# Kernel optimization log

Measured on AMD Instinct MI355X. Metric: run time of the kernel, lower is better.

The kernel has to match this reference:

```python
import jax, jax.numpy as jnp
import numpy as np
import math

B, T, C = 2, 2048, 2048
NH, L = 16, 128  # n_head, LCompression


def setup_inputs() -> dict:
    key = jax.random.key(0)
    ks = jax.random.split(key, 7)
    s = 0.02
    return {
        "x": jax.random.normal(ks[0], (B, T, C), dtype=jnp.float32),
        # latent: Linear(n_embd -> LComp), stored as [in, out]
        "W_lat": jax.random.normal(ks[1], (C, L), dtype=jnp.float32) * s,
        "b_lat": jnp.zeros((L,), dtype=jnp.float32),
        # Wd: Linear(n_embd -> n_head*LComp)
        "W_d": jax.random.normal(ks[2], (C, NH * L), dtype=jnp.float32) * s,
        "b_d": jnp.zeros((NH * L,), dtype=jnp.float32),
        # c_proj: Linear(n_head*LComp -> n_embd)
        "W_proj": jax.random.normal(ks[3], (NH * L, C), dtype=jnp.float32) * s,
        "b_proj": jnp.zeros((C,), dtype=jnp.float32),
    }


def reference(x, W_lat, b_lat, W_d, b_d, W_proj, b_proj):
    Bx, Tx, Cx = x.shape
    # shared low-rank latent, used as both K and V (identical across heads)
    k = x @ W_lat + b_lat                                   # [B,T,L]
    q = (x @ W_d + b_d).reshape(Bx, Tx, NH, L)              # [B,T,H,L]
    q = jnp.transpose(q, (0, 2, 1, 3))                      # [B,H,T,L]
    scale = 1.0 / math.sqrt(L)
    # scores against the head-shared latent (no per-head K expansion)
    att = jnp.einsum("bhtl,bsl->bhts", q, k) * scale        # [B,H,T,T]
    causal = jnp.tril(jnp.ones((Tx, Tx), dtype=bool))
    att = jnp.where(causal[None, None], att, -jnp.inf)
    att = jax.nn.softmax(att, axis=-1)
    y = jnp.einsum("bhts,bsl->bhtl", att, k)                # [B,H,T,L]
    y = jnp.transpose(y, (0, 2, 1, 3)).reshape(Bx, Tx, NH * L)
    return y @ W_proj + b_proj                              # [B,T,C]
```

## Files before the change

### kernel.cpp

```cpp
#include <hip/hip_runtime.h>
#include <hip/hip_bf16.h>

#define B_   2
#define T_   2048
#define C_   2048
#define NH_  16
#define L_   128
#define NKQ  2176
#define MTOK 4096
#define SCALE_ 0.08838834764831845f
#define SCALE2_ 0.12753785792696073f

typedef short short8 __attribute__((ext_vector_type(8)));
typedef float f32x4  __attribute__((ext_vector_type(4)));

#define GLD16(gp, lp) __builtin_amdgcn_global_load_lds(                      \
    (const __attribute__((address_space(1))) void*)(gp),                     \
    (__attribute__((address_space(3))) void*)(lp), 16, 0, 0)

__device__ __forceinline__ unsigned short f2bf(float f) {
  union { float f; unsigned u; } x; x.f = f;
  unsigned r = x.u + 0x7fffu + ((x.u >> 16) & 1u);
  return (unsigned short)(r >> 16);
}

__global__ __launch_bounds__(256) void prep_all(
    const float* __restrict__ x, const float* __restrict__ W_lat,
    const float* __restrict__ W_d, const float* __restrict__ W_proj,
    const float* __restrict__ b_lat, const float* __restrict__ b_d,
    unsigned short* __restrict__ x_bf, unsigned short* __restrict__ BtCat,
    unsigned short* __restrict__ WprojT, float* __restrict__ biascat) {
  __shared__ float tile[32][33];
  int bid = blockIdx.x;
  const int tid = threadIdx.x;

  if (bid < 8192) {
    int i = bid * 1024 + tid * 4;
    float4 v = *(const float4*)(x + i);
    ushort4 o;
    o.x = f2bf(v.x); o.y = f2bf(v.y); o.z = f2bf(v.z); o.w = f2bf(v.w);
    *(ushort4*)(x_bf + i) = o;
    return;
  }
  bid -= 8192;

  const float* W; unsigned short* Wt; int K, N; float mul; int nbx;
  if (bid < 256) {
    W = W_lat; Wt = BtCat; K = C_; N = L_; mul = 1.f; nbx = 4;
  } else if (bid < 256 + 4096) {
    bid -= 256;
    W = W_d; Wt = BtCat + (size_t)L_ * C_; K = C_; N = NH_ * L_; mul = SCALE2_; nbx = 64;
  } else if (bid < 256 + 8192) {
    bid -= 256 + 4096;
    W = W_proj; Wt = WprojT; K = NH_ * L_; N = C_; mul = 1.f; nbx = 64;
  } else {
    int i = (bid - (256 + 8192)) * 256 + tid;
    if (i < L_) biascat[i] = b_lat[i];
    else if (i < NKQ) biascat[i] = b_d[i - L_] * SCALE2_;
    return;
  }

  const int bx = (bid % nbx) * 32, by = (bid / nbx) * 32;
  const int tx = tid & 31, ty = tid >> 5;
  #pragma unroll
  for (int i2 = 0; i2 < 4; i2++)
    tile[ty + i2 * 8][tx] = W[(size_t)(by + ty + i2 * 8) * N + bx + tx];
  __syncthreads();
  #pragma unroll
  for (int i2 = 0; i2 < 4; i2++)
    Wt[(size_t)(bx + ty + i2 * 8) * K + by + tx] = f2bf(tile[tx][ty + i2 * 8] * mul);
}

__global__ void transpose_lat(const unsigned short* __restrict__ kq,
                              unsigned short* __restrict__ KlT) {
  __shared__ unsigned short tile[32][33];
  int t0 = blockIdx.x * 32, l0 = blockIdx.y * 32, b = blockIdx.z;
  int tx = threadIdx.x, ty = threadIdx.y;
  #pragma unroll
  for (int i = 0; i < 4; i++)
    tile[ty + i * 8][tx] = kq[((size_t)b * T_ + t0 + ty + i * 8) * NKQ + l0 + tx];
  __syncthreads();
  #pragma unroll
  for (int i = 0; i < 4; i++)
    KlT[((size_t)b * L_ + l0 + ty + i * 8) * T_ + t0 + tx] = tile[tx][ty + i * 8];
}

__global__ __launch_bounds__(256) void gemm_bt_bias(
    const unsigned short* __restrict__ A,
    const unsigned short* __restrict__ Bt,
    const float* __restrict__ bias,
    unsigned short* __restrict__ Cb,
    float* __restrict__ Cf,
    int M, int N, int K) {
  __shared__ __align__(16) unsigned short As[128 * 32];
  __shared__ __align__(16) unsigned short Bs[128 * 32];
  const int tid  = threadIdx.x;
  const int wave = tid >> 6, lane = tid & 63;
  const int lcol = lane & 15, quad = lane >> 4;
  const int m0 = blockIdx.x * 128, n0 = blockIdx.y * 128;
  const int wm = (wave >> 1) * 64, wn = (wave & 1) * 64;
  const int lrow = lane >> 2, lchunk = (lane & 3) * 8;

  f32x4 acc[4][4];
  #pragma unroll
  for (int i = 0; i < 4; i++)
    #pragma unroll
    for (int j = 0; j < 4; j++) acc[i][j] = (f32x4){0.f, 0.f, 0.f, 0.f};

  for (int kc = 0; kc < K; kc += 32) {
    __syncthreads();
    {
      int rb = wave * 32;
      GLD16(&A [(size_t)(m0 + rb      + lrow) * K + kc + lchunk], &As[ rb       * 32]);
      GLD16(&A [(size_t)(m0 + rb + 16 + lrow) * K + kc + lchunk], &As[(rb + 16) * 32]);
      GLD16(&Bt[(size_t)(n0 + rb      + lrow) * K + kc + lchunk], &Bs[ rb       * 32]);
      GLD16(&Bt[(size_t)(n0 + rb + 16 + lrow) * K + kc + lchunk], &Bs[(rb + 16) * 32]);
    }
    __syncthreads();
    short8 af[4], bfr[4];
    #pragma unroll
    for (int i = 0; i < 4; i++)
      af[i] = *(const short8*)&As[(wm + i * 16 + lcol) * 32 + quad * 8];
    #pragma unroll
    for (int j = 0; j < 4; j++)
      bfr[j] = *(const short8*)&Bs[(wn + j * 16 + lcol) * 32 + quad * 8];
    #pragma unroll
    for (int i = 0; i < 4; i++)
      #pragma unroll
      for (int j = 0; j < 4; j++)
        acc[i][j] = __builtin_amdgcn_mfma_f32_16x16x32_bf16(af[i], bfr[j], acc[i][j], 0, 0, 0);
  }

  #pragma unroll
  for (int i = 0; i < 4; i++) {
    #pragma unroll
    for (int j = 0; j < 4; j++) {
      int col = n0 + wn + j * 16 + lcol;
      float bv = bias[col];
      #pragma unroll
      for (int r = 0; r < 4; r++) {
        int row = m0 + wm + i * 16 + quad * 4 + r;
        float v = acc[i][j][r] + bv;
        if (Cf) Cf[(size_t)row * N + col] = v;
        else    Cb[(size_t)row * N + col] = f2bf(v);
      }
    }
  }
}

__global__ __launch_bounds__(256, 2) void attn_mla(
    const unsigned short* __restrict__ kq,
    const unsigned short* __restrict__ KlT,
    unsigned short* __restrict__ y) {
  __shared__ __align__(16) unsigned short Kr[2][64 * 128];
  __shared__ __align__(16) unsigned short Kt[2][128 * 64];
  __shared__ __align__(16) unsigned short Pls[4][32 * 64];

  const int tid  = threadIdx.x;
  const int wave = tid >> 6, lane = tid & 63;
  const int lcol = lane & 15, quad = lane >> 4;
  const int n    = blockIdx.x;
  const int slot = n >> 8, c = n & 255;
  const int hg   = c >> 5, qi = c & 31;
  const int b    = hg >> 2;
  const int h    = (hg & 3) * 4 + wave;
  const int qt32 = slot ? qi : (63 - qi);
  const size_t rowbase = (size_t)b * T_;
  const int q0 = qt32 * 32;
  unsigned short* Pw = &Pls[wave][0];

  short8 qf[2][4];
  #pragma unroll
  for (int i = 0; i < 2; i++) {
    const unsigned short* qp = kq + (rowbase + q0 + i * 16 + lcol) * NKQ + L_ + h * L_;
    #pragma unroll
    for (int kc = 0; kc < 4; kc++)
      qf[i][kc] = *(const short8*)(qp + kc * 32 + quad * 8);
  }

  f32x4 acco[2][8];
  #pragma unroll
  for (int i = 0; i < 2; i++)
    #pragma unroll
    for (int ns = 0; ns < 8; ns++) acco[i][ns] = (f32x4){0.f, 0.f, 0.f, 0.f};
  float lsum[2][4];
  #pragma unroll
  for (int i = 0; i < 2; i++)
    #pragma unroll
    for (int r = 0; r < 4; r++) lsum[i][r] = 0.f;

  const int nt = (qt32 >> 1) + 1;

  #pragma unroll
  for (int kk = 0; kk < 4; kk++) {
    int r0 = wave * 16 + kk * 4;
    int rg = r0 + (lane >> 4);
    int cl = ((lane & 15) ^ (rg & 7)) * 8;
    GLD16(kq + (rowbase + rg) * NKQ + cl, &Kr[0][r0 * 128]);
  }
  #pragma unroll
  for (int kk = 0; kk < 4; kk++) {
    int r0 = wave * 32 + kk * 8;
    int rg = r0 + (lane >> 3);
    int cl = ((lane & 7) ^ (rg & 7)) * 8;
    GLD16(KlT + ((size_t)b * L_ + rg) * T_ + cl, &Kt[0][r0 * 64]);
  }

  for (int ts = 0; ts < nt; ts++) {
    const int cur = ts & 1;
    __syncthreads();

    if (ts + 1 < nt) {
      const int s1 = (ts + 1) * 64;
      #pragma unroll
      for (int kk = 0; kk < 4; kk++) {
        int r0 = wave * 16 + kk * 4;
        int rg = r0 + (lane >> 4);
        int cl = ((lane & 15) ^ (rg & 7)) * 8;
        GLD16(kq + (rowbase + s1 + rg) * NKQ + cl, &Kr[cur ^ 1][r0 * 128]);
      }
      #pragma unroll
      for (int kk = 0; kk < 4; kk++) {
        int r0 = wave * 32 + kk * 8;
        int rg = r0 + (lane >> 3);
        int cl = ((lane & 7) ^ (rg & 7)) * 8;
        GLD16(KlT + ((size_t)b * L_ + rg) * T_ + s1 + cl, &Kt[cur ^ 1][r0 * 64]);
      }
    }

    const unsigned short* Krc = &Kr[cur][0];
    const unsigned short* Ktc = &Kt[cur][0];

    f32x4 accs[2][4];
    #pragma unroll
    for (int i = 0; i < 2; i++)
      #pragma unroll
      for (int ns = 0; ns < 4; ns++) accs[i][ns] = (f32x4){0.f, 0.f, 0.f, 0.f};
    __builtin_amdgcn_s_setprio(1);
    #pragma unroll
    for (int kc = 0; kc < 4; kc++)
      #pragma unroll
      for (int ns = 0; ns < 4; ns++) {
        short8 bfrag = *(const short8*)&Krc[(ns * 16 + lcol) * 128 +
                                            (((kc * 4 + quad) ^ (lcol & 7)) * 8)];
        #pragma unroll
        for (int i = 0; i < 2; i++)
          accs[i][ns] = __builtin_amdgcn_mfma_f32_16x16x32_bf16(qf[i][kc], bfrag, accs[i][ns], 0, 0, 0);
      }
    __builtin_amdgcn_s_setprio(0);

    const bool diag = (ts == nt - 1);
    #pragma unroll
    for (int half = 0; half < 2; half++) {
      #pragma unroll
      for (int i = 0; i < 2; i++)
        #pragma unroll
        for (int n2 = 0; n2 < 2; n2++) {
          const int ns = half * 2 + n2;
          #pragma unroll
          for (int r = 0; r < 4; r++) {
            float v = accs[i][ns][r];
            int sg = ns * 16 + lcol;
            int qg = (qt32 & 1) * 32 + i * 16 + quad * 4 + r;
            if (diag && sg > qg) v = -1e30f;
            float e = __builtin_amdgcn_exp2f(v);
            unsigned eu = __float_as_uint(e) & 0xffff0000u;
            lsum[i][r] += __uint_as_float(eu);
            int row = i * 16 + quad * 4 + r;
            int col = ns * 16 + lcol;
            int phys = ((col >> 3) ^ (row & 7));
            Pw[row * 64 + phys * 8 + (col & 7)] = (unsigned short)(eu >> 16);
          }
        }

      short8 pa[2];
      #pragma unroll
      for (int i = 0; i < 2; i++)
        pa[i] = *(const short8*)&Pw[(i * 16 + lcol) * 64 +
                                    (((half * 4 + quad) ^ (lcol & 7)) * 8)];
      __builtin_amdgcn_s_setprio(1);
      #pragma unroll
      for (int ns = 0; ns < 8; ns++) {
        short8 bfrag = *(const short8*)&Ktc[(ns * 16 + lcol) * 64 +
                                            (((half * 4 + quad) ^ (lcol & 7)) * 8)];
        #pragma unroll
        for (int i = 0; i < 2; i++)
          acco[i][ns] = __builtin_amdgcn_mfma_f32_16x16x32_bf16(pa[i], bfrag, acco[i][ns], 0, 0, 0);
      }
      __builtin_amdgcn_s_setprio(0);
    }
  }

  #pragma unroll
  for (int i = 0; i < 2; i++)
    #pragma unroll
    for (int r = 0; r < 4; r++) {
      float s = lsum[i][r];
      #pragma unroll
      for (int off = 1; off < 16; off <<= 1) s += __shfl_xor(s, off, 64);
      lsum[i][r] = 1.f / s;
    }

  #pragma unroll
  for (int i = 0; i < 2; i++)
    #pragma unroll
    for (int ns = 0; ns < 8; ns++)
      #pragma unroll
      for (int r = 0; r < 4; r++) {
        int qg = q0 + i * 16 + quad * 4 + r;
        y[(rowbase + qg) * (NH_ * L_) + h * L_ + ns * 16 + lcol] =
            f2bf(acco[i][ns][r] * lsum[i][r]);
      }
}

extern "C" void kernel_launch(void* const* d_in, const int* in_sizes, int n_in,
                              void* d_out, int out_size, void* d_ws, size_t ws_size,
                              hipStream_t stream) {
  const float* x      = (const float*)d_in[0];
  const float* W_lat  = (const float*)d_in[1];
  const float* b_lat  = (const float*)d_in[2];
  const float* W_d    = (const float*)d_in[3];
  const float* b_d    = (const float*)d_in[4];
  const float* W_proj = (const float*)d_in[5];
  const float* b_proj = (const float*)d_in[6];
  float* out = (float*)d_out;

  unsigned short* x_bf   = (unsigned short*)d_ws;
  unsigned short* BtCat  = x_bf   + (size_t)MTOK * C_;
  unsigned short* WprojT = BtCat  + (size_t)NKQ * C_;
  unsigned short* kqbuf  = WprojT + (size_t)C_ * (NH_ * L_);
  unsigned short* ybuf   = kqbuf  + (size_t)MTOK * NKQ;
  unsigned short* KlT    = ybuf   + (size_t)MTOK * (NH_ * L_);
  float*          biascat = (float*)(KlT + (size_t)B_ * L_ * T_);

  prep_all<<<16649, 256, 0, stream>>>(x, W_lat, W_d, W_proj, b_lat, b_d,
                                      x_bf, BtCat, WprojT, biascat);
  gemm_bt_bias<<<dim3(MTOK / 128, NKQ / 128), 256, 0, stream>>>(
      x_bf, BtCat, biascat, kqbuf, nullptr, MTOK, NKQ, C_);
  transpose_lat<<<dim3(T_ / 32, L_ / 32, B_), dim3(32, 8), 0, stream>>>(kqbuf, KlT);
  attn_mla<<<512, 256, 0, stream>>>(kqbuf, KlT, ybuf);
  gemm_bt_bias<<<dim3(MTOK / 128, C_ / 128), 256, 0, stream>>>(
      ybuf, WprojT, b_proj, nullptr, out, MTOK, C_, C_);
}
```

Measured before the change: 295.0 us.

## Restructure GEMM with 256x128 tiles, triple-buffered LDS and swizzled layout

Rewrites the bias GEMM to use 512-thread blocks computing 256x128 output tiles with a 64-wide K step, three LDS buffers prefetched two stages ahead, and an XOR-swizzled LDS layout to avoid bank conflicts. The loop waits on vmcnt rather than doing a full sync, and MFMA sections run at raised wave priority. The aim is to overlap global loads with matrix math and cut per-iteration barrier and LDS conflict overhead in both projection GEMMs. LDS use grows to about 144KB per block, which limits occupancy to one block per CU, and the grid shrinks to fewer, larger blocks.

```diff
diff --git a/kernel.cpp b/kernel.cpp
--- a/kernel.cpp
+++ b/kernel.cpp
@@ -85,21 +85,21 @@
     KlT[((size_t)b * L_ + l0 + ty + i * 8) * T_ + t0 + tx] = tile[tx][ty + i * 8];
 }
 
-__global__ __launch_bounds__(256) void gemm_bt_bias(
+__global__ __launch_bounds__(512) void gemm_bt_bias(
     const unsigned short* __restrict__ A,
     const unsigned short* __restrict__ Bt,
     const float* __restrict__ bias,
     unsigned short* __restrict__ Cb,
     float* __restrict__ Cf,
     int M, int N, int K) {
-  __shared__ __align__(16) unsigned short As[128 * 32];
-  __shared__ __align__(16) unsigned short Bs[128 * 32];
+  __shared__ __align__(16) unsigned short As[3][256 * 64];
+  __shared__ __align__(16) unsigned short Bs[3][128 * 64];
   const int tid  = threadIdx.x;
   const int wave = tid >> 6, lane = tid & 63;
   const int lcol = lane & 15, quad = lane >> 4;
-  const int m0 = blockIdx.x * 128, n0 = blockIdx.y * 128;
-  const int wm = (wave >> 1) * 64, wn = (wave & 1) * 64;
-  const int lrow = lane >> 2, lchunk = (lane & 3) * 8;
+  const int wm = wave >> 1, wn = wave & 1;
+  const int m0 = blockIdx.x * 256, n0 = blockIdx.y * 128;
+  const int arow = lane >> 3, achunk = lane & 7;
 
   f32x4 acc[4][4];
   #pragma unroll
@@ -107,40 +107,73 @@
     #pragma unroll
     for (int j = 0; j < 4; j++) acc[i][j] = (f32x4){0.f, 0.f, 0.f, 0.f};
 
-  for (int kc = 0; kc < K; kc += 32) {
-    __syncthreads();
-    {
-      int rb = wave * 32;
-      GLD16(&A [(size_t)(m0 + rb      + lrow) * K + kc + lchunk], &As[ rb       * 32]);
-      GLD16(&A [(size_t)(m0 + rb + 16 + lrow) * K + kc + lchunk], &As[(rb + 16) * 32]);
-      GLD16(&Bt[(size_t)(n0 + rb      + lrow) * K + kc + lchunk], &Bs[ rb       * 32]);
-      GLD16(&Bt[(size_t)(n0 + rb + 16 + lrow) * K + kc + lchunk], &Bs[(rb + 16) * 32]);
-    }
-    __syncthreads();
-    short8 af[4], bfr[4];
-    #pragma unroll
-    for (int i = 0; i < 4; i++)
-      af[i] = *(const short8*)&As[(wm + i * 16 + lcol) * 32 + quad * 8];
-    #pragma unroll
-    for (int j = 0; j < 4; j++)
-      bfr[j] = *(const short8*)&Bs[(wn + j * 16 + lcol) * 32 + quad * 8];
-    #pragma unroll
-    for (int i = 0; i < 4; i++)
-      #pragma unroll
-      for (int j = 0; j < 4; j++)
-        acc[i][j] = __builtin_amdgcn_mfma_f32_16x16x32_bf16(af[i], bfr[j], acc[i][j], 0, 0, 0);
-  }
-
-  #pragma unroll
-  for (int i = 0; i < 4; i++) {
-    #pragma unroll
-    for (int j = 0; j < 4; j++) {
-      int col = n0 + wn + j * 16 + lcol;
+  const int nk = K >> 6;
+
+  auto STAGE = [&](int kt, int buf) {
+    const int kc = kt << 6;
+    #pragma unroll
+    for (int u = 0; u < 4; u++) {
+      int r0 = (wave * 4 + u) * 8;
+      int rg = r0 + arow;
+      int cl = (achunk ^ (rg & 7)) * 8;
+      GLD16(&A[(size_t)(m0 + rg) * K + kc + cl], &As[buf][r0 * 64]);
+    }
+    #pragma unroll
+    for (int u = 0; u < 2; u++) {
+      int r0 = (wave * 2 + u) * 8;
+      int rg = r0 + arow;
+      int cl = (achunk ^ (rg & 7)) * 8;
+      GLD16(&Bt[(size_t)(n0 + rg) * K + kc + cl], &Bs[buf][r0 * 64]);
+    }
+  };
+
+  STAGE(0, 0);
+  STAGE(1, 1);
+
+  for (int kt = 0; kt < nk; ++kt) {
+    const int buf = kt % 3;
+    if (kt + 1 < nk) asm volatile("s_waitcnt vmcnt(6)" ::: "memory");
+    else             asm volatile("s_waitcnt vmcnt(0)" ::: "memory");
+    __builtin_amdgcn_s_barrier();
+    __builtin_amdgcn_sched_barrier(0);
+    if (kt + 2 < nk) STAGE(kt + 2, (kt + 2) % 3);
+
+    short8 af[4][2], bfr[4][2];
+    #pragma unroll
+    for (int m = 0; m < 4; m++)
+      #pragma unroll
+      for (int ks = 0; ks < 2; ks++) {
+        int row = wm * 64 + m * 16 + lcol;
+        af[m][ks] = *(const short8*)&As[buf][row * 64 + (((ks * 4 + quad) ^ (lcol & 7)) * 8)];
+      }
+    #pragma unroll
+    for (int n = 0; n < 4; n++)
+      #pragma unroll
+      for (int ks = 0; ks < 2; ks++) {
+        int row = wn * 64 + n * 16 + lcol;
+        bfr[n][ks] = *(const short8*)&Bs[buf][row * 64 + (((ks * 4 + quad) ^ (lcol & 7)) * 8)];
+      }
+    __builtin_amdgcn_s_setprio(1);
+    #pragma unroll
+    for (int ks = 0; ks < 2; ks++)
+      #pragma unroll
+      for (int m = 0; m < 4; m++)
+        #pragma unroll
+        for (int n = 0; n < 4; n++)
+          acc[m][n] = __builtin_amdgcn_mfma_f32_16x16x32_bf16(af[m][ks], bfr[n][ks], acc[m][n], 0, 0, 0);
+    __builtin_amdgcn_s_setprio(0);
+  }
+
+  #pragma unroll
+  for (int m = 0; m < 4; m++) {
+    #pragma unroll
+    for (int n = 0; n < 4; n++) {
+      int col = n0 + wn * 64 + n * 16 + lcol;
       float bv = bias[col];
       #pragma unroll
       for (int r = 0; r < 4; r++) {
-        int row = m0 + wm + i * 16 + quad * 4 + r;
-        float v = acc[i][j][r] + bv;
+        int row = m0 + wm * 64 + m * 16 + quad * 4 + r;
+        float v = acc[m][n][r] + bv;
         if (Cf) Cf[(size_t)row * N + col] = v;
         else    Cb[(size_t)row * N + col] = f2bf(v);
       }
@@ -335,10 +368,10 @@
 
   prep_all<<<16649, 256, 0, stream>>>(x, W_lat, W_d, W_proj, b_lat, b_d,
                                       x_bf, BtCat, WprojT, biascat);
-  gemm_bt_bias<<<dim3(MTOK / 128, NKQ / 128), 256, 0, stream>>>(
+  gemm_bt_bias<<<dim3(MTOK / 256, NKQ / 128), 512, 0, stream>>>(
       x_bf, BtCat, biascat, kqbuf, nullptr, MTOK, NKQ, C_);
   transpose_lat<<<dim3(T_ / 32, L_ / 32, B_), dim3(32, 8), 0, stream>>>(kqbuf, KlT);
   attn_mla<<<512, 256, 0, stream>>>(kqbuf, KlT, ybuf);
-  gemm_bt_bias<<<dim3(MTOK / 128, C_ / 128), 256, 0, stream>>>(
+  gemm_bt_bias<<<dim3(MTOK / 256, C_ / 128), 512, 0, stream>>>(
       ybuf, WprojT, b_proj, nullptr, out, MTOK, C_, C_);
 }
```

Result: slower. 315.0 us (+6.8%).
